# Performance work log

Measured on AMD Instinct MI355X. Metric: run time of the kernel, lower is better.

The kernel has to match this reference:

```python
import jax, jax.numpy as jnp
import numpy as np

B, S, D, E, H, K = 4, 4096, 256, 8, 512, 2  # batch, seq, d_model, n_experts, ffn_hidden(=2*D), top_k


def setup_inputs() -> dict:
    key = jax.random.key(0)
    ks = jax.random.split(key, 6)
    x = jax.random.normal(ks[0], (B, S, D), jnp.float32)
    Wg = jax.random.normal(ks[1], (D, E), jnp.float32) * 0.02
    bg = jnp.zeros((E,), jnp.float32)
    W1 = jax.random.normal(ks[2], (E, D, H), jnp.float32) * 0.02
    b1 = jnp.zeros((E, H), jnp.float32)
    W2 = jax.random.normal(ks[3], (E, H, D), jnp.float32) * 0.02
    b2 = jnp.zeros((E, D), jnp.float32)
    return {"x": x, "Wg": Wg, "bg": bg, "W1": W1, "b1": b1, "W2": W2, "b2": b2}


def reference(x, Wg, bg, W1, b1, W2, b2):
    Bv, Sv, Dv = x.shape
    # Gate: linear -> top_k indices. NOTE: the original computes softmax(top_k scores)
    # but never uses the probabilities in the combine, so only indices matter.
    gate_scores = x @ Wg + bg                      # [B,S,E]
    _, idx = jax.lax.top_k(gate_scores, K)          # [B,S,K] (distinct experts per token)
    # Boolean membership mask per expert (0/1), matching (expert_indices == i).any(-1)
    mask = jax.nn.one_hot(idx, E, dtype=x.dtype).sum(axis=-2)  # [B,S,E]

    xf = x.reshape(-1, Dv)                          # [T,D]
    mf = mask.reshape(-1, E)                        # [T,E]
    # Dense all-experts FFN, masked combine (faithful to unweighted scatter-add).
    h = jax.nn.gelu(jnp.einsum('td,edh->teh', xf, W1) + b1[None], approximate=False)  # [T,E,H]
    y = jnp.einsum('teh,ehd->ted', h, W2) + b2[None]                                   # [T,E,D]
    out = jnp.einsum('ted,te->td', y, mf)                                              # [T,D]
    return out.reshape(Bv, Sv, Dv)
```

## Files before the change

### kernel.cpp

```cpp
#include <hip/hip_runtime.h>
#include <hip/hip_bf16.h>

#define T_TOK 16384
#define DM 256
#define NE 8
#define HF 512
#define TM 32
#define XS_LD 264

typedef __bf16 bf16x8 __attribute__((ext_vector_type(8)));
typedef float f32x4 __attribute__((ext_vector_type(4)));
typedef unsigned short u16x8 __attribute__((ext_vector_type(8)));

#define MFMA16(a, b, c) __builtin_amdgcn_mfma_f32_16x16x32_bf16((a), (b), (c), 0, 0, 0)

__device__ __forceinline__ unsigned short f2bf(float f) {
  unsigned u = __float_as_uint(f);
  u += 0x7fffu + ((u >> 16) & 1u);
  return (unsigned short)(u >> 16);
}

__device__ __forceinline__ float gelu_f(float v) {
  float s = fabsf(v) * 0.70710678118654752f;
  float t = __builtin_amdgcn_rcpf(1.0f + 0.3275911f * s);
  float p = t * (0.254829592f +
            t * (-0.284496736f +
            t * (1.421413741f +
            t * (-1.453152027f + t * 1.061405429f))));
  float e = 1.0f - p * __expf(-s * s);
  e = copysignf(e, v);
  return 0.5f * v * (1.0f + e);
}

__device__ __forceinline__ void pack_body(const float* __restrict__ in,
                                          unsigned short* __restrict__ out,
                                          int K, int N, int idx) {
  int n = idx & (N - 1);
  int rest = idx / N;
  int kq = rest & ((K >> 3) - 1);
  int eidx = rest / (K >> 3);
  int k0 = kq * 8;
  const float* src = in + ((size_t)eidx * K + k0) * N + n;
  u16x8 pk;
#pragma unroll
  for (int j = 0; j < 8; j++) pk[j] = f2bf(src[(size_t)j * N]);
  size_t baseo = (size_t)eidx * K * N +
                 (size_t)((n >> 4) * (K >> 5) + (k0 >> 5)) * 512 +
                 (size_t)(((k0 >> 3) & 3) * 128 + (n & 15) * 8);
  *reinterpret_cast<u16x8*>(out + baseo) = pk;
}

__global__ __launch_bounds__(256) void prep_kernel(
    const float* __restrict__ W1, const float* __restrict__ W2,
    unsigned short* __restrict__ w1p, unsigned short* __restrict__ w2p,
    const float* __restrict__ x, const float* __restrict__ Wg,
    const float* __restrict__ bg, int* __restrict__ cnts, int* __restrict__ list) {
  __shared__ float wg_s[DM * NE];
  __shared__ int hist[NE], base_s[NE], rank[NE];
  int b = blockIdx.x;
  int tid = threadIdx.x;
  if (b < 512) {
    pack_body(W1, w1p, DM, HF, b * 256 + tid);
    return;
  }
  if (b < 1024) {
    pack_body(W2, w2p, HF, DM, (b - 512) * 256 + tid);
    return;
  }
  int gb = b - 1024;
  {
    float4 wv0 = *reinterpret_cast<const float4*>(Wg + tid * 8);
    float4 wv1 = *reinterpret_cast<const float4*>(Wg + tid * 8 + 4);
    *reinterpret_cast<float4*>(&wg_s[tid * 8]) = wv0;
    *reinterpret_cast<float4*>(&wg_s[tid * 8 + 4]) = wv1;
  }
  if (tid < NE) { hist[tid] = 0; rank[tid] = 0; }
  __syncthreads();

  int tl = tid >> 2;
  int cg = tid & 3;
  int t = gb * 64 + tl;
  const float* xr = x + (size_t)t * DM + cg * 64;
  double acc[NE];
#pragma unroll
  for (int i = 0; i < NE; i++) acc[i] = 0.0;
  for (int d = 0; d < 64; d += 4) {
    float4 xv = *reinterpret_cast<const float4*>(xr + d);
    const float* w0 = &wg_s[(cg * 64 + d) * NE];
    float xa[4] = {xv.x, xv.y, xv.z, xv.w};
#pragma unroll
    for (int dd = 0; dd < 4; dd++) {
      float4 wa = *reinterpret_cast<const float4*>(w0 + dd * NE);
      float4 wb = *reinterpret_cast<const float4*>(w0 + dd * NE + 4);
      double xd = (double)xa[dd];
      acc[0] += xd * (double)wa.x; acc[1] += xd * (double)wa.y;
      acc[2] += xd * (double)wa.z; acc[3] += xd * (double)wa.w;
      acc[4] += xd * (double)wb.x; acc[5] += xd * (double)wb.y;
      acc[6] += xd * (double)wb.z; acc[7] += xd * (double)wb.w;
    }
  }
#pragma unroll
  for (int i = 0; i < NE; i++) {
    acc[i] += __shfl_xor(acc[i], 1, 64);
    acc[i] += __shfl_xor(acc[i], 2, 64);
    acc[i] += (double)bg[i];
  }
  int e1 = 0;
#pragma unroll
  for (int i = 1; i < NE; i++) if (acc[i] > acc[e1]) e1 = i;
  int e2 = -1;
#pragma unroll
  for (int i = 0; i < NE; i++) {
    if (i == e1) continue;
    if (e2 < 0 || acc[i] > acc[e2]) e2 = i;
  }
  if (cg == 0) {
    atomicAdd(&hist[e1], 1);
    atomicAdd(&hist[e2], 1);
  }
  __syncthreads();
  if (tid < NE) base_s[tid] = atomicAdd(&cnts[tid], hist[tid]);
  __syncthreads();
  if (cg == 0) {
    int r1 = atomicAdd(&rank[e1], 1);
    list[e1 * T_TOK + base_s[e1] + r1] = t;
    int r2 = atomicAdd(&rank[e2], 1);
    list[e2 * T_TOK + base_s[e2] + r2] = t;
  }
}

__global__ __launch_bounds__(256, 4) void ffn_kernel(
    const float* __restrict__ x, const unsigned short* __restrict__ w1p,
    const float* __restrict__ b1, const unsigned short* __restrict__ w2p,
    const float* __restrict__ b2, const int* __restrict__ cnts,
    const int* __restrict__ list, float* __restrict__ out) {
  __shared__ unsigned short Xs[TM * XS_LD];
  __shared__ unsigned short Hl[TM * XS_LD];
  __shared__ int tok[TM];

  int e = blockIdx.x & 7;
  int tile = blockIdx.x >> 3;
  int cnt = cnts[e];
  int base = tile * TM;
  if (base >= cnt) return;
  int rowsv = min(TM, cnt - base);

  int tid = threadIdx.x;
  int w = tid >> 6, lane = tid & 63;
  int quad = lane >> 4, l16 = lane & 15;

  const unsigned short* w1e = w1p + (size_t)e * (HF * DM) + lane * 8;
  const unsigned short* w2e = w2p + (size_t)e * (DM * HF) + lane * 8;

  bf16x8 bcur[4];
#pragma unroll
  for (int nt = 0; nt < 4; nt++)
    bcur[nt] = *reinterpret_cast<const bf16x8*>(w1e + (size_t)((w * 4 + nt) * 8) * 512);

  {
    int r = tid >> 3, cg = tid & 7;
    int token = -1;
    if (r < rowsv) token = list[e * T_TOK + base + r];
    if (cg == 0) tok[r] = token;
    unsigned short* xrow = &Xs[r * XS_LD + cg * 32];
    if (token >= 0) {
      const float* xr = x + (size_t)token * DM + cg * 32;
#pragma unroll
      for (int j = 0; j < 8; j++) {
        float4 v = *reinterpret_cast<const float4*>(xr + j * 4);
        unsigned long long pk = (unsigned long long)f2bf(v.x) |
                                ((unsigned long long)f2bf(v.y) << 16) |
                                ((unsigned long long)f2bf(v.z) << 32) |
                                ((unsigned long long)f2bf(v.w) << 48);
        *reinterpret_cast<unsigned long long*>(xrow + j * 4) = pk;
      }
    } else {
#pragma unroll
      for (int j = 0; j < 8; j++)
        *reinterpret_cast<unsigned long long*>(xrow + j * 4) = 0ull;
    }
  }
  __syncthreads();

  f32x4 zero4 = {0.f, 0.f, 0.f, 0.f};
  f32x4 pacc[2][4];

#pragma unroll
  for (int mt = 0; mt < 2; mt++)
#pragma unroll
    for (int nt = 0; nt < 4; nt++) pacc[mt][nt] = zero4;
#pragma unroll
  for (int ks = 0; ks < 8; ks++) {
    bf16x8 bn[4];
#pragma unroll
    for (int nt = 0; nt < 4; nt++) {
      int tn = (ks < 7) ? (w * 4 + nt) : (16 + w * 4 + nt);
      int kk = (ks < 7) ? (ks + 1) : 0;
      bn[nt] = *reinterpret_cast<const bf16x8*>(w1e + (size_t)(tn * 8 + kk) * 512);
    }
    bf16x8 a[2];
#pragma unroll
    for (int mt = 0; mt < 2; mt++)
      a[mt] = *reinterpret_cast<const bf16x8*>(&Xs[(mt * 16 + l16) * XS_LD + ks * 32 + quad * 8]);
#pragma unroll
    for (int nt = 0; nt < 4; nt++)
#pragma unroll
      for (int mt = 0; mt < 2; mt++)
        pacc[mt][nt] = MFMA16(a[mt], bcur[nt], pacc[mt][nt]);
#pragma unroll
    for (int nt = 0; nt < 4; nt++) bcur[nt] = bn[nt];
  }
#pragma unroll
  for (int nt = 0; nt < 4; nt++) {
    float bias1 = b1[e * HF + w * 64 + nt * 16 + l16];
#pragma unroll
    for (int mt = 0; mt < 2; mt++)
#pragma unroll
      for (int r = 0; r < 4; r++) {
        int row = mt * 16 + quad * 4 + r;
        Hl[row * XS_LD + w * 64 + nt * 16 + l16] = f2bf(gelu_f(pacc[mt][nt][r] + bias1));
      }
  }

#pragma unroll
  for (int mt = 0; mt < 2; mt++)
#pragma unroll
    for (int nt = 0; nt < 4; nt++) pacc[mt][nt] = zero4;
#pragma unroll
  for (int ks = 0; ks < 8; ks++) {
    bf16x8 bn[4];
#pragma unroll
    for (int nt = 0; nt < 4; nt++) {
      if (ks < 7) {
        bn[nt] = *reinterpret_cast<const bf16x8*>(
            w1e + (size_t)((16 + w * 4 + nt) * 8 + ks + 1) * 512);
      } else {
        bn[nt] = *reinterpret_cast<const bf16x8*>(w2e + (size_t)((w * 4 + nt) * 16) * 512);
      }
    }
    bf16x8 a[2];
#pragma unroll
    for (int mt = 0; mt < 2; mt++)
      a[mt] = *reinterpret_cast<const bf16x8*>(&Xs[(mt * 16 + l16) * XS_LD + ks * 32 + quad * 8]);
#pragma unroll
    for (int nt = 0; nt < 4; nt++)
#pragma unroll
      for (int mt = 0; mt < 2; mt++)
        pacc[mt][nt] = MFMA16(a[mt], bcur[nt], pacc[mt][nt]);
#pragma unroll
    for (int nt = 0; nt < 4; nt++) bcur[nt] = bn[nt];
  }
  __syncthreads();
#pragma unroll
  for (int nt = 0; nt < 4; nt++) {
    float bias1 = b1[e * HF + 256 + w * 64 + nt * 16 + l16];
#pragma unroll
    for (int mt = 0; mt < 2; mt++)
#pragma unroll
      for (int r = 0; r < 4; r++) {
        int row = mt * 16 + quad * 4 + r;
        Xs[row * XS_LD + w * 64 + nt * 16 + l16] = f2bf(gelu_f(pacc[mt][nt][r] + bias1));
      }
  }
  __syncthreads();

  f32x4 oacc[2][4];
#pragma unroll
  for (int mt = 0; mt < 2; mt++)
#pragma unroll
    for (int nt = 0; nt < 4; nt++) oacc[mt][nt] = zero4;
#pragma unroll
  for (int ks2 = 0; ks2 < 16; ks2++) {
    bf16x8 bn[4];
    if (ks2 < 15) {
#pragma unroll
      for (int nt = 0; nt < 4; nt++)
        bn[nt] = *reinterpret_cast<const bf16x8*>(
            w2e + (size_t)((w * 4 + nt) * 16 + ks2 + 1) * 512);
    }
    const unsigned short* hbase = (ks2 < 8) ? Hl : Xs;
    int col = (ks2 & 7) * 32 + quad * 8;
    bf16x8 a[2];
#pragma unroll
    for (int mt = 0; mt < 2; mt++)
      a[mt] = *reinterpret_cast<const bf16x8*>(&hbase[(mt * 16 + l16) * XS_LD + col]);
#pragma unroll
    for (int nt = 0; nt < 4; nt++)
#pragma unroll
      for (int mt = 0; mt < 2; mt++)
        oacc[mt][nt] = MFMA16(a[mt], bcur[nt], oacc[mt][nt]);
    if (ks2 < 15) {
#pragma unroll
      for (int nt = 0; nt < 4; nt++) bcur[nt] = bn[nt];
    }
  }

  float b2v[4];
#pragma unroll
  for (int nt = 0; nt < 4; nt++) b2v[nt] = b2[e * DM + w * 64 + nt * 16 + l16];
#pragma unroll
  for (int mt = 0; mt < 2; mt++) {
#pragma unroll
    for (int r = 0; r < 4; r++) {
      int m = mt * 16 + quad * 4 + r;
      int token = tok[m];
      if (token < 0) continue;
      float* orow = out + (size_t)token * DM;
#pragma unroll
      for (int nt = 0; nt < 4; nt++) {
        int d = w * 64 + nt * 16 + l16;
        atomicAdd(&orow[d], oacc[mt][nt][r] + b2v[nt]);
      }
    }
  }
}

extern "C" void kernel_launch(void* const* d_in, const int* in_sizes, int n_in,
                              void* d_out, int out_size, void* d_ws, size_t ws_size,
                              hipStream_t stream) {
  (void)in_sizes; (void)n_in; (void)ws_size;
  const float* x  = (const float*)d_in[0];
  const float* Wg = (const float*)d_in[1];
  const float* bg = (const float*)d_in[2];
  const float* W1 = (const float*)d_in[3];
  const float* b1 = (const float*)d_in[4];
  const float* W2 = (const float*)d_in[5];
  const float* b2 = (const float*)d_in[6];
  float* out = (float*)d_out;

  char* ws = (char*)d_ws;
  int* cnts = (int*)ws;
  int* list = (int*)(ws + 256);
  unsigned short* w1p = (unsigned short*)(ws + 256 + 524288);
  unsigned short* w2p = (unsigned short*)(ws + 256 + 524288 + 2097152);

  hipMemsetAsync(cnts, 0, 256, stream);
  hipMemsetAsync(d_out, 0, (size_t)out_size * sizeof(float), stream);

  hipLaunchKernelGGL(prep_kernel, dim3(1280), dim3(256), 0, stream,
                     W1, W2, w1p, w2p, x, Wg, bg, cnts, list);
  hipLaunchKernelGGL(ffn_kernel, dim3(NE * 512), dim3(256), 0, stream,
                     x, w1p, b1, w2p, b2, cnts, list, out);
}
```

Measured before the change: 146.3 us.

## Replace output atomics with per-slot plain stores and a combine pass

Each token's first expert writes straight into the output and its second expert writes into a separate workspace buffer. The second slot is tagged with a high bit in the routing list. A new combine kernel then adds the two buffers, which removes the output memset and the float atomicAdds in the FFN epilogue. In exchange it writes and reads an extra full-size buffer and adds a kernel launch.

New measurement: 135.4 us. 7.4% less time.

```diff
diff --git a/kernel.cpp b/kernel.cpp
--- a/kernel.cpp
+++ b/kernel.cpp
@@ -125,7 +125,7 @@
     int r1 = atomicAdd(&rank[e1], 1);
     list[e1 * T_TOK + base_s[e1] + r1] = t;
     int r2 = atomicAdd(&rank[e2], 1);
-    list[e2 * T_TOK + base_s[e2] + r2] = t;
+    list[e2 * T_TOK + base_s[e2] + r2] = t | (1 << 20);
   }
 }
 
@@ -133,7 +133,8 @@
     const float* __restrict__ x, const unsigned short* __restrict__ w1p,
     const float* __restrict__ b1, const unsigned short* __restrict__ w2p,
     const float* __restrict__ b2, const int* __restrict__ cnts,
-    const int* __restrict__ list, float* __restrict__ out) {
+    const int* __restrict__ list, float* __restrict__ out,
+    float* __restrict__ part1) {
   __shared__ unsigned short Xs[TM * XS_LD];
   __shared__ unsigned short Hl[TM * XS_LD];
   __shared__ int tok[TM];
@@ -159,19 +160,20 @@
 
   {
     int r = tid >> 3, cg = tid & 7;
-    int token = -1;
-    if (r < rowsv) token = list[e * T_TOK + base + r];
-    if (cg == 0) tok[r] = token;
+    int v = -1;
+    if (r < rowsv) v = list[e * T_TOK + base + r];
+    if (cg == 0) tok[r] = v;
     unsigned short* xrow = &Xs[r * XS_LD + cg * 32];
-    if (token >= 0) {
+    if (v >= 0) {
+      int token = v & 0xFFFFF;
       const float* xr = x + (size_t)token * DM + cg * 32;
 #pragma unroll
       for (int j = 0; j < 8; j++) {
-        float4 v = *reinterpret_cast<const float4*>(xr + j * 4);
-        unsigned long long pk = (unsigned long long)f2bf(v.x) |
-                                ((unsigned long long)f2bf(v.y) << 16) |
-                                ((unsigned long long)f2bf(v.z) << 32) |
-                                ((unsigned long long)f2bf(v.w) << 48);
+        float4 vv = *reinterpret_cast<const float4*>(xr + j * 4);
+        unsigned long long pk = (unsigned long long)f2bf(vv.x) |
+                                ((unsigned long long)f2bf(vv.y) << 16) |
+                                ((unsigned long long)f2bf(vv.z) << 32) |
+                                ((unsigned long long)f2bf(vv.w) << 48);
         *reinterpret_cast<unsigned long long*>(xrow + j * 4) = pk;
       }
     } else {
@@ -303,22 +305,37 @@
 #pragma unroll
     for (int r = 0; r < 4; r++) {
       int m = mt * 16 + quad * 4 + r;
-      int token = tok[m];
-      if (token < 0) continue;
-      float* orow = out + (size_t)token * DM;
+      int v = tok[m];
+      if (v < 0) continue;
+      int token = v & 0xFFFFF;
+      float* orow = ((v >> 20) ? part1 : out) + (size_t)token * DM;
 #pragma unroll
       for (int nt = 0; nt < 4; nt++) {
         int d = w * 64 + nt * 16 + l16;
-        atomicAdd(&orow[d], oacc[mt][nt][r] + b2v[nt]);
-      }
-    }
+        orow[d] = oacc[mt][nt][r] + b2v[nt];
+      }
+    }
+  }
+}
+
+__global__ __launch_bounds__(256) void combine_kernel(
+    float* __restrict__ out, const float* __restrict__ part1) {
+  float4* o4 = reinterpret_cast<float4*>(out);
+  const float4* p4 = reinterpret_cast<const float4*>(part1);
+  int i0 = blockIdx.x * 256 + threadIdx.x;
+#pragma unroll
+  for (int j = 0; j < 4; j++) {
+    int i = i0 + j * 262144;
+    float4 a = o4[i], b = p4[i];
+    a.x += b.x; a.y += b.y; a.z += b.z; a.w += b.w;
+    o4[i] = a;
   }
 }
 
 extern "C" void kernel_launch(void* const* d_in, const int* in_sizes, int n_in,
                               void* d_out, int out_size, void* d_ws, size_t ws_size,
                               hipStream_t stream) {
-  (void)in_sizes; (void)n_in; (void)ws_size;
+  (void)in_sizes; (void)n_in; (void)ws_size; (void)out_size;
   const float* x  = (const float*)d_in[0];
   const float* Wg = (const float*)d_in[1];
   const float* bg = (const float*)d_in[2];
@@ -333,12 +350,14 @@
   int* list = (int*)(ws + 256);
   unsigned short* w1p = (unsigned short*)(ws + 256 + 524288);
   unsigned short* w2p = (unsigned short*)(ws + 256 + 524288 + 2097152);
+  float* part1 = (float*)(ws + 256 + 524288 + 2097152 + 2097152);
 
   hipMemsetAsync(cnts, 0, 256, stream);
-  hipMemsetAsync(d_out, 0, (size_t)out_size * sizeof(float), stream);
 
   hipLaunchKernelGGL(prep_kernel, dim3(1280), dim3(256), 0, stream,
                      W1, W2, w1p, w2p, x, Wg, bg, cnts, list);
   hipLaunchKernelGGL(ffn_kernel, dim3(NE * 512), dim3(256), 0, stream,
-                     x, w1p, b1, w2p, b2, cnts, list, out);
-}
+                     x, w1p, b1, w2p, b2, cnts, list, out, part1);
+  hipLaunchKernelGGL(combine_kernel, dim3(1024), dim3(256), 0, stream,
+                     out, part1);
+}
```
